# Kernel tuning notes

Hardware: AMD Instinct MI355X
Metric: run time of the kernel (lower is better)

The kernel has to match this reference:

```python
import jax, jax.numpy as jnp
import numpy as np

B, C, H, W = 2048, 4, 64, 64
K = 3  # shift / patch kernel size


def _l2_normalize(x, axis=-1, eps=1e-12):
    n = jnp.linalg.norm(x, axis=axis, keepdims=True)
    return x / jnp.maximum(n, eps)


def _circular_convolution(weights, kernel):
    # weights: [B,H,W], kernel: [B,3,3] (softmax-normalized shift kernel)
    res = jnp.zeros_like(weights)
    c = K // 2
    for dh in range(K):
        for dw in range(K):
            coeff = kernel[:, dh, dw][:, None, None]
            res = res + coeff * jnp.roll(weights, shift=(dh - c, dw - c), axis=(1, 2))
    return res


def _apply_patch(weights, patch):
    # weights: [B,H,W], patch: [B,C,3,3] -> [B,C,H,W]; zero-padded (non-circular) shifts
    c = K // 2
    wp = jnp.pad(weights, ((0, 0), (c, c), (c, c)))  # [B,H+2,W+2]
    res = jnp.zeros((weights.shape[0], patch.shape[1], H, W), dtype=weights.dtype)
    for dh in range(K):
        for dw in range(K):
            coeff = patch[:, :, dh, dw][:, :, None, None]  # [B,C,1,1]
            # result[y,x] += patch[dh,dw] * weights[y-(dh-c), x-(dw-c)] within bounds
            win = wp[:, 2 * c - dh:2 * c - dh + H, 2 * c - dw:2 * c - dw + W]  # [B,H,W]
            res = res + coeff * win[:, None, :, :]
    return res


def setup_inputs() -> dict:
    key = jax.random.key(0)
    ks = jax.random.split(key, 12)
    return {
        "map_state": jax.random.uniform(ks[0], (B, C, H, W), dtype=jnp.float32),
        "weight_state": jnp.ones((B, H, W), dtype=jnp.float32) / float(H * W),
        "key": jax.random.normal(ks[1], (B, C), dtype=jnp.float32),
        "beta": jax.random.normal(ks[2], (B, 1), dtype=jnp.float32),
        "gate": jax.random.normal(ks[3], (B, 1), dtype=jnp.float32),
        "shift": jax.random.normal(ks[4], (B, K * K), dtype=jnp.float32),
        "sharpen": jax.random.normal(ks[5], (B, 1), dtype=jnp.float32),
        "erase": jax.random.normal(ks[6], (B, C), dtype=jnp.float32),
        "add": jax.random.normal(ks[7], (B, C), dtype=jnp.float32),
        "add_patch_logits": jax.random.normal(ks[8], (B, C, K, K), dtype=jnp.float32),
        "erase_patch_logits": jax.random.normal(ks[9], (B, C, K, K), dtype=jnp.float32),
    }


def reference(map_state, weight_state, key, beta, gate, shift, sharpen, erase, add,
              add_patch_logits, erase_patch_logits):
    b = map_state.shape[0]
    # content addressing: cosine similarity against flattened memory
    flat_mem = map_state.reshape(b, C, H * W).transpose(0, 2, 1)  # [B,HW,C]
    key_norm = _l2_normalize(key)                                  # [B,C]
    mem_norm = _l2_normalize(flat_mem)                             # [B,HW,C]
    similarity = jnp.einsum('bnc,bc->bn', mem_norm, key_norm)      # [B,HW]
    beta_pos = jax.nn.softplus(beta) + 1e-6                        # [B,1]
    content_w = jax.nn.softmax(beta_pos * similarity, axis=-1)
    # interpolation gate with previous weights
    gate_sigma = jax.nn.sigmoid(gate)                              # [B,1]
    prev_w = weight_state.reshape(b, -1)
    gated = gate_sigma * content_w + (1.0 - gate_sigma) * prev_w
    # differentiable circular shift
    shift_kernel = jax.nn.softmax(shift, axis=-1).reshape(b, K, K)
    shifted = _circular_convolution(gated.reshape(b, H, W), shift_kernel)
    # sharpening
    sharpen_pos = 1.0 + jax.nn.softplus(sharpen)                   # [B,1]
    sharpened = jnp.clip(shifted, 1e-6, None).reshape(b, -1) ** sharpen_pos
    weights = sharpened / (jnp.sum(sharpened, axis=-1, keepdims=True) + 1e-6)
    weights = weights / (jnp.sum(weights, axis=-1, keepdims=True) + 1e-6)
    weights_2d = weights.reshape(b, H, W)
    # patch-based write (add + erase)
    add_patch = jax.nn.sigmoid(add_patch_logits)
    erase_patch = jax.nn.sigmoid(erase_patch_logits)
    add_map = _apply_patch(weights_2d, add_patch)
    erase_map = jnp.clip(_apply_patch(weights_2d, erase_patch), 0.0, 1.0)
    map_updated = map_state * (1.0 - erase_map) + add_map
    read_vector = jnp.sum(map_updated * weights_2d[:, None, :, :], axis=(2, 3))  # [B,C]
    return map_updated, weights_2d, read_vector
```

## Files before the change

### kernel.cpp

```cpp
#include <hip/hip_runtime.h>
#include <math.h>

#define CC 4
#define HH 64
#define WW 64
#define NN (HH*WW)
#define NTH 256
#define GRP 4
#define NW (NTH/64)
#define LDW 65

#if __has_builtin(__builtin_amdgcn_exp2f)
#define FEXP2(x) __builtin_amdgcn_exp2f(x)
#else
#define FEXP2(x) exp2f(x)
#endif
#if __has_builtin(__builtin_amdgcn_logf)
#define FLOG2(x) __builtin_amdgcn_logf(x)
#else
#define FLOG2(x) log2f(x)
#endif
#define LOG2E  1.4426950408889634f
#define RLOG2E 0.6931471805599453f

__device__ __forceinline__ float fast_softplus(float x) {
    return (x > 20.f) ? x : FLOG2(1.f + FEXP2(x * LOG2E)) * RLOG2E;
}
__device__ __forceinline__ float fast_sigmoid(float x) {
    return 1.f / (1.f + FEXP2(-x * LOG2E));
}

__device__ __forceinline__ float bred_sum(float v, float* sc) {
#pragma unroll
    for (int o = 32; o > 0; o >>= 1) v += __shfl_down(v, o, 64);
    if ((threadIdx.x & 63) == 0) sc[threadIdx.x >> 6] = v;
    __syncthreads();
    return (sc[0] + sc[1]) + (sc[2] + sc[3]);
}

__global__ __launch_bounds__(NTH)
void slam_kernel(const float* __restrict__ map_state,
                 const float* __restrict__ weight_state,
                 const float* __restrict__ key,
                 const float* __restrict__ beta,
                 const float* __restrict__ gate,
                 const float* __restrict__ shift,
                 const float* __restrict__ sharpen,
                 const float* __restrict__ add_patch_logits,
                 const float* __restrict__ erase_patch_logits,
                 float* __restrict__ out_map,
                 float* __restrict__ out_w,
                 float* __restrict__ out_rv)
{
    __shared__ float sw[HH * LDW];
    __shared__ float sp[HH * LDW];
    __shared__ float spatch[2 * CC * 9];
    __shared__ float sks[9];
    __shared__ float sscal[8];
    __shared__ float sred[6][NW];

    const int b = blockIdx.x;
    const int tid = threadIdx.x;

    const float4* mp4 = (const float4*)(map_state    + (size_t)b * CC * NN);
    const float4* pw4 = (const float4*)(weight_state + (size_t)b * NN);
    float4*       om4 = (float4*)(out_map + (size_t)b * CC * NN);
    float4*       ow4 = (float4*)(out_w   + (size_t)b * NN);
    float4*       sp4 = (float4*)sp;

    float4 pwst[GRP];
#pragma unroll
    for (int gix = 0; gix < GRP; ++gix) pwst[gix] = pw4[tid + gix * NTH];

    if (tid == 0) {
        const float* sh = shift + b * 9;
        float m = sh[0];
#pragma unroll
        for (int i = 1; i < 9; ++i) m = fmaxf(m, sh[i]);
        float e[9]; float s = 0.f;
#pragma unroll
        for (int i = 0; i < 9; ++i) { e[i] = FEXP2((sh[i] - m) * LOG2E); s += e[i]; }
        float inv = 1.f / s;
#pragma unroll
        for (int i = 0; i < 9; ++i) sks[i] = e[i] * inv;
    } else if (tid == 64) {
        const float* kb = key + b * CC;
        float a = kb[0], c = kb[1], d = kb[2], f = kb[3];
        float inv = rsqrtf(fmaxf(a*a + c*c + d*d + f*f, 1e-24f));
        sscal[0] = a*inv; sscal[1] = c*inv; sscal[2] = d*inv; sscal[3] = f*inv;
    } else if (tid == 128) {
        sscal[4] = fast_softplus(beta[b]) + 1e-6f;
    } else if (tid == 129) {
        sscal[5] = fast_sigmoid(gate[b]);
    } else if (tid == 130) {
        sscal[6] = 1.f + fast_softplus(sharpen[b]);
    }
    if (tid >= 184) {
        const int i = tid - 184;
        float v = (i < CC * 9) ? add_patch_logits[b * CC * 9 + i]
                               : erase_patch_logits[b * CC * 9 + (i - CC * 9)];
        spatch[i] = fast_sigmoid(v);
    }
#pragma unroll
    for (int gix = 0; gix < GRP; ++gix) sp4[tid + gix * NTH] = pwst[gix];
    __syncthreads();

    const float k0 = sscal[0], k1 = sscal[1], k2 = sscal[2], k3 = sscal[3];
    const float beta_pos = sscal[4], g = sscal[5], sharp_pos = sscal[6];
    const float bL = beta_pos * LOG2E;

    float lsum = 0.f;
#pragma unroll 2
    for (int gix = 0; gix < GRP; ++gix) {
        const int base = tid + gix * NTH;
        const int P = 4 * base, h = P >> 6, w0 = P & 63;
        float4 mv0 = mp4[base];
        float4 mv1 = mp4[(NN/4) + base];
        float4 mv2 = mp4[2*(NN/4) + base];
        float4 mv3 = mp4[3*(NN/4) + base];
        float* row = sw + h * LDW + w0;
#pragma unroll
        for (int j = 0; j < 4; ++j) {
            float a0 = ((const float*)&mv0)[j];
            float a1 = ((const float*)&mv1)[j];
            float a2 = ((const float*)&mv2)[j];
            float a3 = ((const float*)&mv3)[j];
            float inv = rsqrtf(fmaxf(a0*a0 + a1*a1 + a2*a2 + a3*a3, 1e-24f));
            float e = FEXP2(bL * (a0*k0 + a1*k1 + a2*k2 + a3*k3) * inv);
            row[j] = e;
            lsum += e;
        }
    }
    const float Z = bred_sum(lsum, sred[0]);
    const float gZinv = g / Z;
    const float g1 = 1.f - g;

#pragma unroll
    for (int gix = 0; gix < GRP; ++gix) {
        const int base = tid + gix * NTH;
        const int P = 4 * base, h = P >> 6, w0 = P & 63;
        float4 pw = sp4[base];
        float* row = sw + h * LDW + w0;
#pragma unroll
        for (int j = 0; j < 4; ++j)
            row[j] = gZinv * row[j] + g1 * ((const float*)&pw)[j];
    }
    __syncthreads();

    float lsum1 = 0.f;
#pragma unroll
    for (int gix = 0; gix < GRP; ++gix) {
        const int base = tid + gix * NTH;
        const int P = 4 * base, h = P >> 6, w0 = P & 63;
        const int rr[3] = { (h + 1) & 63, h, (h + 63) & 63 };
        const int cm = (w0 + 63) & 63, cp = (w0 + 4) & 63;
        float acc0 = 0.f, acc1 = 0.f, acc2 = 0.f, acc3 = 0.f;
#pragma unroll
        for (int dh = 0; dh < 3; ++dh) {
            const float* rp = sw + rr[dh] * LDW;
            float b0 = rp[cm];
            float b1 = rp[w0];
            float b2 = rp[w0 + 1];
            float b3 = rp[w0 + 2];
            float b4 = rp[w0 + 3];
            float b5 = rp[cp];
            float s0 = sks[dh*3+0], s1 = sks[dh*3+1], s2 = sks[dh*3+2];
            acc0 += s0*b2 + s1*b1 + s2*b0;
            acc1 += s0*b3 + s1*b2 + s2*b1;
            acc2 += s0*b4 + s1*b3 + s2*b2;
            acc3 += s0*b5 + s1*b4 + s2*b3;
        }
        float* prow = sp + h * LDW + w0;
        float p0 = FEXP2(sharp_pos * FLOG2(fmaxf(acc0, 1e-6f)));
        float p1 = FEXP2(sharp_pos * FLOG2(fmaxf(acc1, 1e-6f)));
        float p2 = FEXP2(sharp_pos * FLOG2(fmaxf(acc2, 1e-6f)));
        float p3 = FEXP2(sharp_pos * FLOG2(fmaxf(acc3, 1e-6f)));
        prow[0] = p0; prow[1] = p1; prow[2] = p2; prow[3] = p3;
        lsum1 += (p0 + p1) + (p2 + p3);
    }
    const float S1 = bred_sum(lsum1, sred[1]);
    const float inv1  = 1.f / (S1 + 1e-6f);
    const float S2    = S1 * inv1;
    const float scale = inv1 / (S2 + 1e-6f);

    float rv0 = 0.f, rv1 = 0.f, rv2 = 0.f, rv3 = 0.f;
#pragma unroll 1
    for (int gix = 0; gix < GRP; ++gix) {
        const int base = tid + gix * NTH;
        const int P = 4 * base, h = P >> 6, w0 = P & 63;
        float buf[3][6];
#pragma unroll
        for (int dh = 0; dh < 3; ++dh) {
            const int r = h + 1 - dh;
            if ((unsigned)r < (unsigned)HH) {
                const float* rp = sp + r * LDW;
                buf[dh][0] = (w0 > 0) ? rp[w0 - 1] * scale : 0.f;
                buf[dh][1] = rp[w0]     * scale;
                buf[dh][2] = rp[w0 + 1] * scale;
                buf[dh][3] = rp[w0 + 2] * scale;
                buf[dh][4] = rp[w0 + 3] * scale;
                buf[dh][5] = (w0 + 4 < WW) ? rp[w0 + 4] * scale : 0.f;
            } else {
#pragma unroll
                for (int k = 0; k < 6; ++k) buf[dh][k] = 0.f;
            }
        }
        const float wn0 = buf[1][1], wn1 = buf[1][2], wn2 = buf[1][3], wn3 = buf[1][4];
        {
            float4 o;
            ((float*)&o)[0] = wn0; ((float*)&o)[1] = wn1;
            ((float*)&o)[2] = wn2; ((float*)&o)[3] = wn3;
            ow4[base] = o;
        }
#pragma unroll
        for (int ch = 0; ch < CC; ++ch) {
            float4 m4 = mp4[ch * (NN/4) + base];
            float a0 = 0.f, a1 = 0.f, a2 = 0.f, a3 = 0.f;
            float e0 = 0.f, e1 = 0.f, e2 = 0.f, e3 = 0.f;
#pragma unroll
            for (int dh = 0; dh < 3; ++dh) {
#pragma unroll
                for (int t = 0; t < 3; ++t) {
                    const float ca = spatch[ch * 9 + dh * 3 + t];
                    const float ce = spatch[CC * 9 + ch * 9 + dh * 3 + t];
                    a0 += ca * buf[dh][2 - t];  e0 += ce * buf[dh][2 - t];
                    a1 += ca * buf[dh][3 - t];  e1 += ce * buf[dh][3 - t];
                    a2 += ca * buf[dh][4 - t];  e2 += ce * buf[dh][4 - t];
                    a3 += ca * buf[dh][5 - t];  e3 += ce * buf[dh][5 - t];
                }
            }
            float4 o;
            float mu, acc;
            mu = ((const float*)&m4)[0] * (1.f - fminf(fmaxf(e0, 0.f), 1.f)) + a0;
            ((float*)&o)[0] = mu; acc  = mu * wn0;
            mu = ((const float*)&m4)[1] * (1.f - fminf(fmaxf(e1, 0.f), 1.f)) + a1;
            ((float*)&o)[1] = mu; acc += mu * wn1;
            mu = ((const float*)&m4)[2] * (1.f - fminf(fmaxf(e2, 0.f), 1.f)) + a2;
            ((float*)&o)[2] = mu; acc += mu * wn2;
            mu = ((const float*)&m4)[3] * (1.f - fminf(fmaxf(e3, 0.f), 1.f)) + a3;
            ((float*)&o)[3] = mu; acc += mu * wn3;
            om4[ch * (NN/4) + base] = o;
            if      (ch == 0) rv0 += acc;
            else if (ch == 1) rv1 += acc;
            else if (ch == 2) rv2 += acc;
            else              rv3 += acc;
        }
    }

#pragma unroll
    for (int c = 0; c < CC; ++c) {
        float v = (c == 0) ? rv0 : (c == 1) ? rv1 : (c == 2) ? rv2 : rv3;
#pragma unroll
        for (int o = 32; o > 0; o >>= 1) v += __shfl_down(v, o, 64);
        if ((tid & 63) == 0) sred[2 + c][tid >> 6] = v;
    }
    __syncthreads();
    if (tid < CC) {
        out_rv[(size_t)b * CC + tid] =
            (sred[2 + tid][0] + sred[2 + tid][1]) + (sred[2 + tid][2] + sred[2 + tid][3]);
    }
}

extern "C" void kernel_launch(void* const* d_in, const int* in_sizes, int n_in,
                              void* d_out, int out_size, void* d_ws, size_t ws_size,
                              hipStream_t stream) {
    const float* map_state          = (const float*)d_in[0];
    const float* weight_state       = (const float*)d_in[1];
    const float* key                = (const float*)d_in[2];
    const float* beta               = (const float*)d_in[3];
    const float* gate               = (const float*)d_in[4];
    const float* shift              = (const float*)d_in[5];
    const float* sharpen            = (const float*)d_in[6];
    const float* add_patch_logits   = (const float*)d_in[9];
    const float* erase_patch_logits = (const float*)d_in[10];

    const int B = in_sizes[1] / NN;

    float* out_map = (float*)d_out;
    float* out_w   = out_map + (size_t)B * CC * NN;
    float* out_rv  = out_w   + (size_t)B * NN;

    slam_kernel<<<B, NTH, 0, stream>>>(map_state, weight_state, key, beta, gate,
                                       shift, sharpen, add_patch_logits,
                                       erase_patch_logits, out_map, out_w, out_rv);
}
```

Measured before the change: 87.88 us.

## Double block size, drop second LDS buffer, keep previous weights in registers

Raises the block from 256 to 512 threads, with two float4 groups per thread instead of four. Removes the separate shared buffer for sharpened weights: previous weights stay in registers, and the normalized weights are written back into the single shared map. The weight output is now stored in that extra pass. The aim is to halve LDS use per block and add threads, so more waves are resident to hide memory latency in this bandwidth-bound kernel. The cost is one extra block barrier and wider 8-wave reductions.

```diff
diff --git a/kernel.cpp b/kernel.cpp
--- a/kernel.cpp
+++ b/kernel.cpp
@@ -5,8 +5,8 @@
 #define HH 64
 #define WW 64
 #define NN (HH*WW)
-#define NTH 256
-#define GRP 4
+#define NTH 512
+#define GRP 2
 #define NW (NTH/64)
 #define LDW 65
 
@@ -35,7 +35,9 @@
     for (int o = 32; o > 0; o >>= 1) v += __shfl_down(v, o, 64);
     if ((threadIdx.x & 63) == 0) sc[threadIdx.x >> 6] = v;
     __syncthreads();
-    return (sc[0] + sc[1]) + (sc[2] + sc[3]);
+    float r = ((sc[0] + sc[1]) + (sc[2] + sc[3]))
+            + ((sc[4] + sc[5]) + (sc[6] + sc[7]));
+    return r;
 }
 
 __global__ __launch_bounds__(NTH)
@@ -53,7 +55,6 @@
                  float* __restrict__ out_rv)
 {
     __shared__ float sw[HH * LDW];
-    __shared__ float sp[HH * LDW];
     __shared__ float spatch[2 * CC * 9];
     __shared__ float sks[9];
     __shared__ float sscal[8];
@@ -66,11 +67,9 @@
     const float4* pw4 = (const float4*)(weight_state + (size_t)b * NN);
     float4*       om4 = (float4*)(out_map + (size_t)b * CC * NN);
     float4*       ow4 = (float4*)(out_w   + (size_t)b * NN);
-    float4*       sp4 = (float4*)sp;
-
-    float4 pwst[GRP];
-#pragma unroll
-    for (int gix = 0; gix < GRP; ++gix) pwst[gix] = pw4[tid + gix * NTH];
+
+    float4 pw0 = pw4[tid];
+    float4 pw1 = pw4[tid + NTH];
 
     if (tid == 0) {
         const float* sh = shift + b * 9;
@@ -90,27 +89,25 @@
         sscal[0] = a*inv; sscal[1] = c*inv; sscal[2] = d*inv; sscal[3] = f*inv;
     } else if (tid == 128) {
         sscal[4] = fast_softplus(beta[b]) + 1e-6f;
-    } else if (tid == 129) {
+    } else if (tid == 192) {
         sscal[5] = fast_sigmoid(gate[b]);
-    } else if (tid == 130) {
+    } else if (tid == 256) {
         sscal[6] = 1.f + fast_softplus(sharpen[b]);
     }
-    if (tid >= 184) {
-        const int i = tid - 184;
+    if (tid >= NTH - 72) {
+        const int i = tid - (NTH - 72);
         float v = (i < CC * 9) ? add_patch_logits[b * CC * 9 + i]
                                : erase_patch_logits[b * CC * 9 + (i - CC * 9)];
         spatch[i] = fast_sigmoid(v);
     }
-#pragma unroll
-    for (int gix = 0; gix < GRP; ++gix) sp4[tid + gix * NTH] = pwst[gix];
     __syncthreads();
 
     const float k0 = sscal[0], k1 = sscal[1], k2 = sscal[2], k3 = sscal[3];
-    const float beta_pos = sscal[4], g = sscal[5], sharp_pos = sscal[6];
-    const float bL = beta_pos * LOG2E;
+    const float g = sscal[5], sharp_pos = sscal[6];
+    const float bL = sscal[4] * LOG2E;
 
     float lsum = 0.f;
-#pragma unroll 2
+#pragma unroll 1
     for (int gix = 0; gix < GRP; ++gix) {
         const int base = tid + gix * NTH;
         const int P = 4 * base, h = P >> 6, w0 = P & 63;
@@ -139,7 +136,7 @@
     for (int gix = 0; gix < GRP; ++gix) {
         const int base = tid + gix * NTH;
         const int P = 4 * base, h = P >> 6, w0 = P & 63;
-        float4 pw = sp4[base];
+        const float4 pw = (gix == 0) ? pw0 : pw1;
         float* row = sw + h * LDW + w0;
 #pragma unroll
         for (int j = 0; j < 4; ++j)
@@ -147,8 +144,9 @@
     }
     __syncthreads();
 
+    float z[8];
     float lsum1 = 0.f;
-#pragma unroll
+#pragma unroll 1
     for (int gix = 0; gix < GRP; ++gix) {
         const int base = tid + gix * NTH;
         const int P = 4 * base, h = P >> 6, w0 = P & 63;
@@ -170,19 +168,33 @@
             acc2 += s0*b4 + s1*b3 + s2*b2;
             acc3 += s0*b5 + s1*b4 + s2*b3;
         }
-        float* prow = sp + h * LDW + w0;
-        float p0 = FEXP2(sharp_pos * FLOG2(fmaxf(acc0, 1e-6f)));
-        float p1 = FEXP2(sharp_pos * FLOG2(fmaxf(acc1, 1e-6f)));
-        float p2 = FEXP2(sharp_pos * FLOG2(fmaxf(acc2, 1e-6f)));
-        float p3 = FEXP2(sharp_pos * FLOG2(fmaxf(acc3, 1e-6f)));
-        prow[0] = p0; prow[1] = p1; prow[2] = p2; prow[3] = p3;
-        lsum1 += (p0 + p1) + (p2 + p3);
+        z[gix*4+0] = FEXP2(sharp_pos * FLOG2(fmaxf(acc0, 1e-6f)));
+        z[gix*4+1] = FEXP2(sharp_pos * FLOG2(fmaxf(acc1, 1e-6f)));
+        z[gix*4+2] = FEXP2(sharp_pos * FLOG2(fmaxf(acc2, 1e-6f)));
+        z[gix*4+3] = FEXP2(sharp_pos * FLOG2(fmaxf(acc3, 1e-6f)));
+        lsum1 += (z[gix*4+0] + z[gix*4+1]) + (z[gix*4+2] + z[gix*4+3]);
     }
     const float S1 = bred_sum(lsum1, sred[1]);
     const float inv1  = 1.f / (S1 + 1e-6f);
     const float S2    = S1 * inv1;
     const float scale = inv1 / (S2 + 1e-6f);
 
+#pragma unroll
+    for (int gix = 0; gix < GRP; ++gix) {
+        const int base = tid + gix * NTH;
+        const int P = 4 * base, h = P >> 6, w0 = P & 63;
+        float* row = sw + h * LDW + w0;
+        float4 o;
+#pragma unroll
+        for (int j = 0; j < 4; ++j) {
+            float wv = z[gix*4 + j] * scale;
+            row[j] = wv;
+            ((float*)&o)[j] = wv;
+        }
+        ow4[base] = o;
+    }
+    __syncthreads();
+
     float rv0 = 0.f, rv1 = 0.f, rv2 = 0.f, rv3 = 0.f;
 #pragma unroll 1
     for (int gix = 0; gix < GRP; ++gix) {
@@ -193,25 +205,19 @@
         for (int dh = 0; dh < 3; ++dh) {
             const int r = h + 1 - dh;
             if ((unsigned)r < (unsigned)HH) {
-                const float* rp = sp + r * LDW;
-                buf[dh][0] = (w0 > 0) ? rp[w0 - 1] * scale : 0.f;
-                buf[dh][1] = rp[w0]     * scale;
-                buf[dh][2] = rp[w0 + 1] * scale;
-                buf[dh][3] = rp[w0 + 2] * scale;
-                buf[dh][4] = rp[w0 + 3] * scale;
-                buf[dh][5] = (w0 + 4 < WW) ? rp[w0 + 4] * scale : 0.f;
+                const float* rp = sw + r * LDW;
+                buf[dh][0] = (w0 > 0) ? rp[w0 - 1] : 0.f;
+                buf[dh][1] = rp[w0];
+                buf[dh][2] = rp[w0 + 1];
+                buf[dh][3] = rp[w0 + 2];
+                buf[dh][4] = rp[w0 + 3];
+                buf[dh][5] = (w0 + 4 < WW) ? rp[w0 + 4] : 0.f;
             } else {
 #pragma unroll
                 for (int k = 0; k < 6; ++k) buf[dh][k] = 0.f;
             }
         }
         const float wn0 = buf[1][1], wn1 = buf[1][2], wn2 = buf[1][3], wn3 = buf[1][4];
-        {
-            float4 o;
-            ((float*)&o)[0] = wn0; ((float*)&o)[1] = wn1;
-            ((float*)&o)[2] = wn2; ((float*)&o)[3] = wn3;
-            ow4[base] = o;
-        }
 #pragma unroll
         for (int ch = 0; ch < CC; ++ch) {
             float4 m4 = mp4[ch * (NN/4) + base];
@@ -256,8 +262,10 @@
     }
     __syncthreads();
     if (tid < CC) {
-        out_rv[(size_t)b * CC + tid] =
-            (sred[2 + tid][0] + sred[2 + tid][1]) + (sred[2 + tid][2] + sred[2 + tid][3]);
+        float s = 0.f;
+#pragma unroll
+        for (int i = 0; i < NW; ++i) s += sred[2 + tid][i];
+        out_rv[(size_t)b * CC + tid] = s;
     }
 }
 
```

New measurement: 97.95 us. +11.5%, slower.
